# Kernel optimization log

Hardware: AMD Instinct MI355X
Metric: run time of the kernel (lower is better)

Reference implementation:

```python
import jax, jax.numpy as jnp
import numpy as np

ITERATIONS = 3
OUT_CAPS, OUT_DIM = 10, 16


def squash(x):
    # square_norm / (1 + square_norm) * x / (sqrt(square_norm) + 1e-6), norm over last axis
    sn = jnp.sum(x * x, axis=-1, keepdims=True)
    return sn / (1.0 + sn) * x / (jnp.sqrt(sn) + 1e-6)


def setup_inputs() -> dict:
    key = jax.random.key(0)
    kx, kw = jax.random.split(key)
    x = jax.random.normal(kx, (256, 32, 6, 6, 8), dtype=jnp.float32)
    W = 0.01 * jax.random.normal(kw, (1, 32, 6, 6, 10, 8, 16), dtype=jnp.float32)
    return {"x": x, "W": W}


def reference(x, W):
    w = W[0]  # [i,j,k,o,d,e]
    # u_hat: prediction vectors, [B, i, j, k, O, E]
    u_hat = jnp.einsum('bijkd,ijkode->bijkoe', x, w)
    u_det = jax.lax.stop_gradient(u_hat)
    b = jnp.zeros(u_hat.shape[:-1], dtype=u_hat.dtype)  # [B,i,j,k,O]
    for _ in range(ITERATIONS - 1):
        c = jax.nn.softmax(b, axis=-1)
        s = jnp.einsum('bijko,bijkoe->boe', c, u_det)   # reduce over all input-capsule axes
        v = squash(s)                                    # [B,O,E]
        b = b + jnp.einsum('bijkoe,boe->bijko', u_det, v)
    c = jax.nn.softmax(b, axis=-1)
    s = jnp.einsum('bijko,bijkoe->boe', c, u_hat)
    v = squash(s)
    return v.reshape(-1, OUT_CAPS, OUT_DIM)
```

## Files before the change

kernel.cpp:

```cpp
#include <hip/hip_runtime.h>
#include <math.h>

#define BATCH 256
#define IC    1152
#define DD    8
#define OO    10
#define EE    16
#define BTILE 64
#define NBT   4
#define NT    640
#define CHUNK 9
#define NCHUNK 128

__global__ __launch_bounds__(NT) void caps_pass_kernel(
    const float* __restrict__ x,
    const float* __restrict__ W,
    const float* __restrict__ V,
    float* __restrict__ s_part,
    int first)
{
    __shared__ float x_lds[CHUNK][DD][BTILE];
    __shared__ float elg_lds[CHUNK][NT];

    const int tid = threadIdx.x;
    const int o   = tid >> 6;
    const int bl  = tid & 63;
    const int o_u = __builtin_amdgcn_readfirstlane(o);
    const int b   = blockIdx.y * BTILE + bl;
    const int ijk0 = blockIdx.x * CHUNK;

    {
        const float* xgrp = x + (size_t)(blockIdx.y * BTILE) * (IC * DD);
        #pragma unroll 1
        for (int i = tid; i < CHUNK * BTILE * 2; i += NT) {
            const int lq = i & 1;
            const int lb = (i >> 1) & 63;
            const int ls = i >> 7;
            const float4 t = *reinterpret_cast<const float4*>(
                xgrp + (size_t)lb * (IC * DD) + (size_t)(ijk0 + ls) * DD + lq * 4);
            x_lds[ls][lq * 4 + 0][lb] = t.x;
            x_lds[ls][lq * 4 + 1][lb] = t.y;
            x_lds[ls][lq * 4 + 2][lb] = t.z;
            x_lds[ls][lq * 4 + 3][lb] = t.w;
        }
    }
    __syncthreads();

    if (!first) {
        float vreg[EE];
        const float4* vp = reinterpret_cast<const float4*>(V + ((size_t)b * OO + o) * EE);
        #pragma unroll
        for (int q = 0; q < 4; ++q) {
            float4 t = vp[q];
            vreg[q * 4 + 0] = t.x; vreg[q * 4 + 1] = t.y;
            vreg[q * 4 + 2] = t.z; vreg[q * 4 + 3] = t.w;
        }

        #pragma unroll 1
        for (int s = 0; s < CHUNK; ++s) {
            const float* wp = W + (size_t)(ijk0 + s) * (OO * DD * EE) + o_u * (DD * EE);
            float xr[DD];
            #pragma unroll
            for (int d = 0; d < DD; ++d) xr[d] = x_lds[s][d][bl];
            float lg = 0.f;
            #pragma unroll
            for (int d = 0; d < DD; ++d) {
                float t = 0.f;
                #pragma unroll
                for (int e = 0; e < EE; ++e)
                    t = fmaf(wp[d * EE + e], vreg[e], t);
                lg = fmaf(xr[d], t, lg);
            }
            elg_lds[s][tid] = __expf(lg);
        }
        __syncthreads();
    }

    float sacc[EE];
    #pragma unroll
    for (int e = 0; e < EE; ++e) sacc[e] = 0.f;

    #pragma unroll 1
    for (int s = 0; s < CHUNK; ++s) {
        const float* wp = W + (size_t)(ijk0 + s) * (OO * DD * EE) + o_u * (DD * EE);
        float xr[DD];
        #pragma unroll
        for (int d = 0; d < DD; ++d) xr[d] = x_lds[s][d][bl];

        float c;
        if (!first) {
            float den = 0.f;
            #pragma unroll
            for (int oo = 0; oo < OO; ++oo)
                den += elg_lds[s][oo * 64 + bl];
            c = __fdividef(elg_lds[s][o * 64 + bl], den);
        } else {
            c = 1.0f;
        }

        #pragma unroll
        for (int d = 0; d < DD; ++d) {
            const float cx = c * xr[d];
            #pragma unroll
            for (int e = 0; e < EE; ++e)
                sacc[e] = fmaf(cx, wp[d * EE + e], sacc[e]);
        }
    }

    const float mul = first ? 0.1f : 1.0f;
    float* sp = s_part + (((size_t)blockIdx.x * BATCH + b) * OO + o) * EE;
    #pragma unroll
    for (int q = 0; q < 4; ++q) {
        float4 t;
        t.x = mul * sacc[q * 4 + 0]; t.y = mul * sacc[q * 4 + 1];
        t.z = mul * sacc[q * 4 + 2]; t.w = mul * sacc[q * 4 + 3];
        reinterpret_cast<float4*>(sp)[q] = t;
    }
}

__global__ __launch_bounds__(256) void caps_squash_kernel(
    const float* __restrict__ s_part,
    float* __restrict__ V,
    float* __restrict__ out,
    int accum, int last)
{
    __shared__ float red[3][64];
    const int lane = threadIdx.x & 63;
    const int w    = threadIdx.x >> 6;
    const int g    = blockIdx.x * 64 + lane;

    const float* sp = s_part + g;
    float s = 0.f;
    #pragma unroll 8
    for (int ch = w * (NCHUNK / 4); ch < (w + 1) * (NCHUNK / 4); ++ch)
        s += sp[(size_t)ch * (BATCH * OO * EE)];

    if (w > 0) red[w - 1][lane] = s;
    __syncthreads();
    if (w == 0) {
        s += red[0][lane] + red[1][lane] + red[2][lane];

        float sq = s * s;
        #pragma unroll
        for (int m = 1; m < 16; m <<= 1) sq += __shfl_xor(sq, m, 16);

        float scale = sq / (1.f + sq) / (sqrtf(sq) + 1e-6f);
        float v = scale * s;

        if (last)       out[g] = v;
        else if (accum) V[g]  += v;
        else            V[g]   = v;
    }
}

extern "C" void kernel_launch(void* const* d_in, const int* in_sizes, int n_in,
                              void* d_out, int out_size, void* d_ws, size_t ws_size,
                              hipStream_t stream) {
    const float* x = (const float*)d_in[0];
    const float* W = (const float*)d_in[1];
    float* out = (float*)d_out;

    float* s_part = (float*)d_ws;
    float* V      = s_part + (size_t)NCHUNK * BATCH * OO * EE;

    dim3 grid(NCHUNK, NBT), blk(NT);
    const int sq_blocks = (BATCH * OO * EE) / 64;

    caps_pass_kernel<<<grid, blk, 0, stream>>>(x, W, V, s_part, 1);
    caps_squash_kernel<<<sq_blocks, 256, 0, stream>>>(s_part, V, out, 0, 0);
    caps_pass_kernel<<<grid, blk, 0, stream>>>(x, W, V, s_part, 0);
    caps_squash_kernel<<<sq_blocks, 256, 0, stream>>>(s_part, V, out, 1, 0);
    caps_pass_kernel<<<grid, blk, 0, stream>>>(x, W, V, s_part, 0);
    caps_squash_kernel<<<sq_blocks, 256, 0, stream>>>(s_part, V, out, 0, 1);
}
```

Measured before the change: 158.6 us.

## Compute u_hat once per capsule and reuse it for logits and weighted sum

```diff
diff --git a/kernel.cpp b/kernel.cpp
--- a/kernel.cpp
+++ b/kernel.cpp
@@ -20,7 +20,8 @@
     int first)
 {
     __shared__ float x_lds[CHUNK][DD][BTILE];
-    __shared__ float elg_lds[CHUNK][NT];
+    __shared__ float v_lds[OO][EE][BTILE];
+    __shared__ float elg_lds[2][NT];
 
     const int tid = threadIdx.x;
     const int o   = tid >> 6;
@@ -44,67 +45,62 @@
             x_lds[ls][lq * 4 + 3][lb] = t.w;
         }
     }
-    __syncthreads();
 
     if (!first) {
-        float vreg[EE];
         const float4* vp = reinterpret_cast<const float4*>(V + ((size_t)b * OO + o) * EE);
         #pragma unroll
         for (int q = 0; q < 4; ++q) {
-            float4 t = vp[q];
-            vreg[q * 4 + 0] = t.x; vreg[q * 4 + 1] = t.y;
-            vreg[q * 4 + 2] = t.z; vreg[q * 4 + 3] = t.w;
+            const float4 t = vp[q];
+            v_lds[o][q * 4 + 0][bl] = t.x;
+            v_lds[o][q * 4 + 1][bl] = t.y;
+            v_lds[o][q * 4 + 2][bl] = t.z;
+            v_lds[o][q * 4 + 3][bl] = t.w;
         }
-
-        #pragma unroll 1
-        for (int s = 0; s < CHUNK; ++s) {
-            const float* wp = W + (size_t)(ijk0 + s) * (OO * DD * EE) + o_u * (DD * EE);
-            float xr[DD];
-            #pragma unroll
-            for (int d = 0; d < DD; ++d) xr[d] = x_lds[s][d][bl];
-            float lg = 0.f;
-            #pragma unroll
-            for (int d = 0; d < DD; ++d) {
-                float t = 0.f;
-                #pragma unroll
-                for (int e = 0; e < EE; ++e)
-                    t = fmaf(wp[d * EE + e], vreg[e], t);
-                lg = fmaf(xr[d], t, lg);
-            }
-            elg_lds[s][tid] = __expf(lg);
-        }
-        __syncthreads();
     }
+    __syncthreads();
 
     float sacc[EE];
     #pragma unroll
     for (int e = 0; e < EE; ++e) sacc[e] = 0.f;
 
+    int p = 0;
     #pragma unroll 1
     for (int s = 0; s < CHUNK; ++s) {
         const float* wp = W + (size_t)(ijk0 + s) * (OO * DD * EE) + o_u * (DD * EE);
-        float xr[DD];
+
+        float u[EE];
         #pragma unroll
-        for (int d = 0; d < DD; ++d) xr[d] = x_lds[s][d][bl];
+        for (int e = 0; e < EE; ++e) u[e] = 0.f;
+        #pragma unroll
+        for (int d = 0; d < DD; ++d) {
+            const float xv = x_lds[s][d][bl];
+            #pragma unroll
+            for (int e = 0; e < EE; ++e)
+                u[e] = fmaf(xv, wp[d * EE + e], u[e]);
+        }
 
         float c;
         if (!first) {
+            float lg = 0.f;
+            #pragma unroll
+            for (int e = 0; e < EE; ++e)
+                lg = fmaf(u[e], v_lds[o][e][bl], lg);
+            const float elg = __expf(lg);
+            elg_lds[p][tid] = elg;
+            __syncthreads();
             float den = 0.f;
             #pragma unroll
             for (int oo = 0; oo < OO; ++oo)
-                den += elg_lds[s][oo * 64 + bl];
-            c = __fdividef(elg_lds[s][o * 64 + bl], den);
+                den += elg_lds[p][oo * 64 + bl];
+            c = __fdividef(elg, den);
+            p ^= 1;
         } else {
             c = 1.0f;
         }
 
         #pragma unroll
-        for (int d = 0; d < DD; ++d) {
-            const float cx = c * xr[d];
-            #pragma unroll
-            for (int e = 0; e < EE; ++e)
-                sacc[e] = fmaf(cx, wp[d * EE + e], sacc[e]);
-        }
+        for (int e = 0; e < EE; ++e)
+            sacc[e] = fmaf(c, u[e], sacc[e]);
     }
 
     const float mul = first ? 0.1f : 1.0f;
```

After: 166.3 us. +4.9%, slower.
